# Kernel optimization log

Measured on AMD Instinct MI355X. Metric: run time of the kernel, lower is better.

The kernel has to match this reference:

```python
import jax, jax.numpy as jnp
import numpy as np

N_NODES = 100000
N_EDGES = 3200000
D_IN = 128
D_H0 = 64
D_H1 = 32
N_GRAPHS = 1024
N_CLASSES = 16


def setup_inputs() -> dict:
    key = jax.random.key(0)
    ks = jax.random.split(key, 9)
    x = jax.random.normal(ks[0], (N_NODES, D_IN), dtype=jnp.float32)
    edge_index = jax.random.randint(ks[1], (2, N_EDGES), 0, N_NODES, dtype=jnp.int64)
    node_graph_index = jnp.sort(
        jax.random.randint(ks[2], (N_NODES,), 0, N_GRAPHS, dtype=jnp.int64))

    def glorot(k, shape):
        lim = np.sqrt(6.0 / (shape[0] + shape[1]))
        return jax.random.uniform(k, shape, jnp.float32, -lim, lim)

    W0 = glorot(ks[3], (D_IN, D_H0))
    b0 = jnp.zeros((D_H0,), jnp.float32)
    W1 = glorot(ks[4], (D_H0, D_H1))
    b1 = jnp.zeros((D_H1,), jnp.float32)
    Wd = glorot(ks[5], (D_H1, N_CLASSES))
    bd = jnp.zeros((N_CLASSES,), jnp.float32)
    return {"x": x, "edge_index": edge_index, "node_graph_index": node_graph_index,
            "W0": W0, "b0": b0, "W1": W1, "b1": b1, "Wd": Wd, "bd": bd}


def reference(x, edge_index, node_graph_index, W0, b0, W1, b1, Wd, bd):
    N = x.shape[0]
    # GCN renormalization: add self-loops, symmetric D^-1/2 (A+I) D^-1/2
    loops = jnp.arange(N, dtype=edge_index.dtype)
    row = jnp.concatenate([edge_index[0], loops])  # target nodes
    col = jnp.concatenate([edge_index[1], loops])  # source nodes
    deg = jax.ops.segment_sum(jnp.ones_like(row, dtype=x.dtype), row, num_segments=N)
    inv_sqrt = jax.lax.rsqrt(deg)  # deg >= 1 thanks to self-loops
    norm = inv_sqrt[row] * inv_sqrt[col]  # [E+N]

    def gcn(h, W, b):
        hW = h @ W                                   # [N, d_out]
        msg = hW[col] * norm[:, None]                # [E+N, d_out]
        agg = jax.ops.segment_sum(msg, row, num_segments=N)
        return jax.nn.relu(agg + b)

    h = gcn(x, W0, b0)          # [N, 64]  (dropout is identity at inference)
    h = gcn(h, W1, b1)          # [N, 32]

    # mean pool over graphs
    sums = jax.ops.segment_sum(h, node_graph_index, num_segments=N_GRAPHS)
    cnt = jax.ops.segment_sum(jnp.ones((N,), x.dtype), node_graph_index,
                              num_segments=N_GRAPHS)
    pooled = sums / jnp.maximum(cnt, 1.0)[:, None]   # [G, 32]
    return pooled @ Wd + bd                          # [G, n_classes]
```

## Files before the change

### kernel.cpp

```cpp
#include <hip/hip_runtime.h>

#define GSHIFT 8
#define GSIZE 256
#define MAXG 512
#define GCAP 8960
#define CHUNKA 4096

typedef unsigned short bfraw;

__device__ __forceinline__ bfraw f2bf(float f) {
    unsigned u = __float_as_uint(f);
    unsigned r = u + 0x7FFFu + ((u >> 16) & 1u);
    return (bfraw)(r >> 16);
}
__device__ __forceinline__ float bflo(unsigned u) { return __uint_as_float(u << 16); }
__device__ __forceinline__ float bfhi(unsigned u) { return __uint_as_float(u & 0xFFFF0000u); }


__global__ __launch_bounds__(512) void k_ginit(int* __restrict__ gcur, int ngroups) {
    int g = threadIdx.x;
    if (g < ngroups) gcur[g] = g * GCAP;
}

__global__ __launch_bounds__(512) void k_partA(const int* __restrict__ row,
                                               const int* __restrict__ col,
                                               int* __restrict__ gcur,
                                               int* __restrict__ gbuf,
                                               int E, int ngroups) {
    __shared__ int h[MAXG];
    __shared__ int lst[MAXG];
    __shared__ int base[MAXG];
    __shared__ int sorted[CHUNKA];
    __shared__ int dstIdx[CHUNKA];
    int tid = threadIdx.x;
    h[tid] = 0;
    __syncthreads();
    int start = blockIdx.x * CHUNKA;
    int end = min(E, start + CHUNKA);
    for (int i = start + tid * 4; i < end; i += 2048) {
        if (i + 3 < end) {
            int4 r = *(const int4*)(row + i);
            atomicAdd(&h[r.x >> GSHIFT], 1);
            atomicAdd(&h[r.y >> GSHIFT], 1);
            atomicAdd(&h[r.z >> GSHIFT], 1);
            atomicAdd(&h[r.w >> GSHIFT], 1);
        } else {
            for (int j = i; j < end; ++j) atomicAdd(&h[row[j] >> GSHIFT], 1);
        }
    }
    __syncthreads();
    int v = h[tid];
    lst[tid] = v;
    __syncthreads();
    for (int d = 1; d < MAXG; d <<= 1) {
        int a = (tid >= d) ? lst[tid - d] : 0;
        __syncthreads();
        lst[tid] += a;
        __syncthreads();
    }
    int excl = lst[tid] - v;
    base[tid] = (v > 0 && tid < ngroups) ? atomicAdd(&gcur[tid], v) : 0;
    lst[tid] = excl;
    h[tid] = excl;
    __syncthreads();
    for (int i = start + tid * 4; i < end; i += 2048) {
        if (i + 3 < end) {
            int4 r = *(const int4*)(row + i);
            int4 c = *(const int4*)(col + i);
#pragma unroll
            for (int j = 0; j < 4; ++j) {
                int rr = (&r.x)[j], cc = (&c.x)[j];
                int g = rr >> GSHIFT;
                int p = atomicAdd(&h[g], 1);
                sorted[p] = ((rr & (GSIZE - 1)) << 17) | cc;
                int dst = base[g] + (p - lst[g]);
                dstIdx[p] = (dst < (g + 1) * GCAP) ? dst : -1;
            }
        } else {
            for (int j = i; j < end; ++j) {
                int rr = row[j], cc = col[j];
                int g = rr >> GSHIFT;
                int p = atomicAdd(&h[g], 1);
                sorted[p] = ((rr & (GSIZE - 1)) << 17) | cc;
                int dst = base[g] + (p - lst[g]);
                dstIdx[p] = (dst < (g + 1) * GCAP) ? dst : -1;
            }
        }
    }
    __syncthreads();
    int cnt = end - start;
    for (int i = tid; i < cnt; i += 512) {
        int d = dstIdx[i];
        if (d >= 0) gbuf[d] = sorted[i];
    }
}

__global__ __launch_bounds__(512) void k_partB(const int* __restrict__ gbuf,
                                               const int* __restrict__ gcur,
                                               int* __restrict__ off,
                                               int* __restrict__ off2,
                                               int* __restrict__ scol,
                                               float* __restrict__ invs, int N) {
    __shared__ int hist[GSIZE];
    __shared__ int lex[GSIZE];
    __shared__ int sorted[GCAP];
    int g = blockIdx.x, tid = threadIdx.x;
    int s = g * GCAP;
    int cnt = min(gcur[g] - s, GCAP);
    if (tid < GSIZE) hist[tid] = 0;
    __syncthreads();
    for (int k = tid; k < cnt; k += 512)
        atomicAdd(&hist[gbuf[s + k] >> 17], 1);
    __syncthreads();
    int d0 = (tid < GSIZE) ? hist[tid] : 0;
    if (tid < GSIZE) lex[tid] = d0;
    __syncthreads();
    for (int d = 1; d < GSIZE; d <<= 1) {
        int a = 0;
        if (tid < GSIZE && tid >= d) a = lex[tid - d];
        __syncthreads();
        if (tid < GSIZE) lex[tid] += a;
        __syncthreads();
    }
    if (tid < GSIZE) {
        int excl = lex[tid] - d0;
        int node = (g << GSHIFT) + tid;
        if (node < N) {
            off[node] = s + excl;
            off2[node] = s + excl + d0;
            invs[node] = rsqrtf((float)(d0 + 1));
        }
        hist[tid] = excl;
    }
    __syncthreads();
    for (int k = tid; k < cnt; k += 512) {
        int p = gbuf[s + k];
        int pos = atomicAdd(&hist[p >> 17], 1);
        sorted[pos] = p & 0x1FFFF;
    }
    __syncthreads();
    for (int k = tid; k < cnt; k += 512) scol[s + k] = sorted[k];
}


__global__ __launch_bounds__(256) void k_gemm0(const float* __restrict__ x,
                                               const float* __restrict__ W,
                                               const float* __restrict__ invs,
                                               bfraw* __restrict__ out, int N) {
    __shared__ float sW[128 * 64];
    for (int i = threadIdx.x; i < 2048; i += 256)
        ((float4*)sW)[i] = ((const float4*)W)[i];
    __syncthreads();
    int t = threadIdx.x;
    int tc = t & 15, tr = t >> 4;
    int rbase = blockIdx.x * 64 + tr * 4;
    float acc[4][4] = {};
    int rr[4];
#pragma unroll
    for (int i = 0; i < 4; ++i) rr[i] = min(rbase + i, N - 1);
    for (int k = 0; k < 128; k += 4) {
        float4 wv0 = *(const float4*)&sW[(k + 0) * 64 + tc * 4];
        float4 wv1 = *(const float4*)&sW[(k + 1) * 64 + tc * 4];
        float4 wv2 = *(const float4*)&sW[(k + 2) * 64 + tc * 4];
        float4 wv3 = *(const float4*)&sW[(k + 3) * 64 + tc * 4];
#pragma unroll
        for (int i = 0; i < 4; ++i) {
            float4 xv = *(const float4*)(x + (size_t)rr[i] * 128 + k);
            acc[i][0] = fmaf(xv.x, wv0.x, acc[i][0]);
            acc[i][1] = fmaf(xv.x, wv0.y, acc[i][1]);
            acc[i][2] = fmaf(xv.x, wv0.z, acc[i][2]);
            acc[i][3] = fmaf(xv.x, wv0.w, acc[i][3]);
            acc[i][0] = fmaf(xv.y, wv1.x, acc[i][0]);
            acc[i][1] = fmaf(xv.y, wv1.y, acc[i][1]);
            acc[i][2] = fmaf(xv.y, wv1.z, acc[i][2]);
            acc[i][3] = fmaf(xv.y, wv1.w, acc[i][3]);
            acc[i][0] = fmaf(xv.z, wv2.x, acc[i][0]);
            acc[i][1] = fmaf(xv.z, wv2.y, acc[i][1]);
            acc[i][2] = fmaf(xv.z, wv2.z, acc[i][2]);
            acc[i][3] = fmaf(xv.z, wv2.w, acc[i][3]);
            acc[i][0] = fmaf(xv.w, wv3.x, acc[i][0]);
            acc[i][1] = fmaf(xv.w, wv3.y, acc[i][1]);
            acc[i][2] = fmaf(xv.w, wv3.z, acc[i][2]);
            acc[i][3] = fmaf(xv.w, wv3.w, acc[i][3]);
        }
    }
#pragma unroll
    for (int i = 0; i < 4; ++i) {
        int row = rbase + i;
        if (row < N) {
            float iv = invs[row];
            ushort4 o;
            o.x = f2bf(iv * acc[i][0]);
            o.y = f2bf(iv * acc[i][1]);
            o.z = f2bf(iv * acc[i][2]);
            o.w = f2bf(iv * acc[i][3]);
            *(ushort4*)(out + (size_t)row * 64 + tc * 4) = o;
        }
    }
}

__global__ __launch_bounds__(256) void k_gemm1(const float* __restrict__ h,
                                               const float* __restrict__ W,
                                               const float* __restrict__ invs,
                                               bfraw* __restrict__ out, int N) {
    __shared__ float sW[64 * 32];
    for (int i = threadIdx.x; i < 512; i += 256)
        ((float4*)sW)[i] = ((const float4*)W)[i];
    __syncthreads();
    int t = threadIdx.x;
    int tc = t & 7, tr = t >> 3;
    int rbase = blockIdx.x * 128 + tr * 4;
    float acc[4][4] = {};
    int rr[4];
#pragma unroll
    for (int i = 0; i < 4; ++i) rr[i] = min(rbase + i, N - 1);
    for (int k = 0; k < 64; k += 4) {
        float4 wv0 = *(const float4*)&sW[(k + 0) * 32 + tc * 4];
        float4 wv1 = *(const float4*)&sW[(k + 1) * 32 + tc * 4];
        float4 wv2 = *(const float4*)&sW[(k + 2) * 32 + tc * 4];
        float4 wv3 = *(const float4*)&sW[(k + 3) * 32 + tc * 4];
#pragma unroll
        for (int i = 0; i < 4; ++i) {
            float4 xv = *(const float4*)(h + (size_t)rr[i] * 64 + k);
            acc[i][0] = fmaf(xv.x, wv0.x, acc[i][0]);
            acc[i][1] = fmaf(xv.x, wv0.y, acc[i][1]);
            acc[i][2] = fmaf(xv.x, wv0.z, acc[i][2]);
            acc[i][3] = fmaf(xv.x, wv0.w, acc[i][3]);
            acc[i][0] = fmaf(xv.y, wv1.x, acc[i][0]);
            acc[i][1] = fmaf(xv.y, wv1.y, acc[i][1]);
            acc[i][2] = fmaf(xv.y, wv1.z, acc[i][2]);
            acc[i][3] = fmaf(xv.y, wv1.w, acc[i][3]);
            acc[i][0] = fmaf(xv.z, wv2.x, acc[i][0]);
            acc[i][1] = fmaf(xv.z, wv2.y, acc[i][1]);
            acc[i][2] = fmaf(xv.z, wv2.z, acc[i][2]);
            acc[i][3] = fmaf(xv.z, wv2.w, acc[i][3]);
            acc[i][0] = fmaf(xv.w, wv3.x, acc[i][0]);
            acc[i][1] = fmaf(xv.w, wv3.y, acc[i][1]);
            acc[i][2] = fmaf(xv.w, wv3.z, acc[i][2]);
            acc[i][3] = fmaf(xv.w, wv3.w, acc[i][3]);
        }
    }
#pragma unroll
    for (int i = 0; i < 4; ++i) {
        int row = rbase + i;
        if (row < N) {
            float iv = invs[row];
            ushort4 o;
            o.x = f2bf(iv * acc[i][0]);
            o.y = f2bf(iv * acc[i][1]);
            o.z = f2bf(iv * acc[i][2]);
            o.w = f2bf(iv * acc[i][3]);
            *(ushort4*)(out + (size_t)row * 32 + tc * 4) = o;
        }
    }
}


__global__ __launch_bounds__(256) void k_agg64_w(const int* __restrict__ scol,
                                                 const int* __restrict__ off,
                                                 const int* __restrict__ off2,
                                                 const float* __restrict__ invs,
                                                 const bfraw* __restrict__ hWb,
                                                 const float* __restrict__ bias,
                                                 float* __restrict__ h0, int N) {
    int node = blockIdx.x * 4 + (threadIdx.x >> 6);
    if (node >= N) return;
    int lane = threadIdx.x & 63;
    int fl = lane & 7, sg = lane >> 3;
    int s = off[node], e = off2[node];
    float a[8] = {}, c[8] = {};
    int k = s + sg;
    for (; k + 24 < e; k += 32) {
        int n0 = scol[k], n1 = scol[k + 8], n2 = scol[k + 16], n3 = scol[k + 24];
        uint4 u0 = *(const uint4*)(hWb + (size_t)n0 * 64 + fl * 8);
        uint4 u1 = *(const uint4*)(hWb + (size_t)n1 * 64 + fl * 8);
        uint4 u2 = *(const uint4*)(hWb + (size_t)n2 * 64 + fl * 8);
        uint4 u3 = *(const uint4*)(hWb + (size_t)n3 * 64 + fl * 8);
        a[0] += bflo(u0.x); a[1] += bfhi(u0.x); a[2] += bflo(u0.y); a[3] += bfhi(u0.y);
        a[4] += bflo(u0.z); a[5] += bfhi(u0.z); a[6] += bflo(u0.w); a[7] += bfhi(u0.w);
        c[0] += bflo(u1.x); c[1] += bfhi(u1.x); c[2] += bflo(u1.y); c[3] += bfhi(u1.y);
        c[4] += bflo(u1.z); c[5] += bfhi(u1.z); c[6] += bflo(u1.w); c[7] += bfhi(u1.w);
        a[0] += bflo(u2.x); a[1] += bfhi(u2.x); a[2] += bflo(u2.y); a[3] += bfhi(u2.y);
        a[4] += bflo(u2.z); a[5] += bfhi(u2.z); a[6] += bflo(u2.w); a[7] += bfhi(u2.w);
        c[0] += bflo(u3.x); c[1] += bfhi(u3.x); c[2] += bflo(u3.y); c[3] += bfhi(u3.y);
        c[4] += bflo(u3.z); c[5] += bfhi(u3.z); c[6] += bflo(u3.w); c[7] += bfhi(u3.w);
    }
    for (; k < e; k += 8) {
        uint4 u = *(const uint4*)(hWb + (size_t)scol[k] * 64 + fl * 8);
        a[0] += bflo(u.x); a[1] += bfhi(u.x); a[2] += bflo(u.y); a[3] += bfhi(u.y);
        a[4] += bflo(u.z); a[5] += bfhi(u.z); a[6] += bflo(u.w); a[7] += bfhi(u.w);
    }
#pragma unroll
    for (int j = 0; j < 8; ++j) a[j] += c[j];
#pragma unroll
    for (int m = 8; m < 64; m <<= 1) {
#pragma unroll
        for (int j = 0; j < 8; ++j) a[j] += __shfl_xor(a[j], m, 64);
    }
    if (sg == 0) {
        uint4 u = *(const uint4*)(hWb + (size_t)node * 64 + fl * 8);
        float iv = invs[node];
        int fb = fl * 8;
        float4 o1, o2;
        o1.x = fmaxf(iv * (a[0] + bflo(u.x)) + bias[fb + 0], 0.f);
        o1.y = fmaxf(iv * (a[1] + bfhi(u.x)) + bias[fb + 1], 0.f);
        o1.z = fmaxf(iv * (a[2] + bflo(u.y)) + bias[fb + 2], 0.f);
        o1.w = fmaxf(iv * (a[3] + bfhi(u.y)) + bias[fb + 3], 0.f);
        o2.x = fmaxf(iv * (a[4] + bflo(u.z)) + bias[fb + 4], 0.f);
        o2.y = fmaxf(iv * (a[5] + bfhi(u.z)) + bias[fb + 5], 0.f);
        o2.z = fmaxf(iv * (a[6] + bflo(u.w)) + bias[fb + 6], 0.f);
        o2.w = fmaxf(iv * (a[7] + bfhi(u.w)) + bias[fb + 7], 0.f);
        *(float4*)(h0 + (size_t)node * 64 + fb) = o1;
        *(float4*)(h0 + (size_t)node * 64 + fb + 4) = o2;
    }
}

__global__ __launch_bounds__(256) void k_agg32_w(const int* __restrict__ scol,
                                                 const int* __restrict__ off,
                                                 const int* __restrict__ off2,
                                                 const float* __restrict__ invs,
                                                 const bfraw* __restrict__ hWb,
                                                 const float* __restrict__ bias,
                                                 float* __restrict__ h1, int N) {
    int node = blockIdx.x * 4 + (threadIdx.x >> 6);
    if (node >= N) return;
    int lane = threadIdx.x & 63;
    int fl = lane & 3, sg = lane >> 2;
    int s = off[node], e = off2[node];
    float a[8] = {}, c[8] = {};
    int k = s + sg;
    for (; k + 16 < e; k += 32) {
        int n0 = scol[k], n1 = scol[k + 16];
        uint4 u0 = *(const uint4*)(hWb + (size_t)n0 * 32 + fl * 8);
        uint4 u1 = *(const uint4*)(hWb + (size_t)n1 * 32 + fl * 8);
        a[0] += bflo(u0.x); a[1] += bfhi(u0.x); a[2] += bflo(u0.y); a[3] += bfhi(u0.y);
        a[4] += bflo(u0.z); a[5] += bfhi(u0.z); a[6] += bflo(u0.w); a[7] += bfhi(u0.w);
        c[0] += bflo(u1.x); c[1] += bfhi(u1.x); c[2] += bflo(u1.y); c[3] += bfhi(u1.y);
        c[4] += bflo(u1.z); c[5] += bfhi(u1.z); c[6] += bflo(u1.w); c[7] += bfhi(u1.w);
    }
    for (; k < e; k += 16) {
        uint4 u = *(const uint4*)(hWb + (size_t)scol[k] * 32 + fl * 8);
        a[0] += bflo(u.x); a[1] += bfhi(u.x); a[2] += bflo(u.y); a[3] += bfhi(u.y);
        a[4] += bflo(u.z); a[5] += bfhi(u.z); a[6] += bflo(u.w); a[7] += bfhi(u.w);
    }
#pragma unroll
    for (int j = 0; j < 8; ++j) a[j] += c[j];
#pragma unroll
    for (int m = 4; m < 64; m <<= 1) {
#pragma unroll
        for (int j = 0; j < 8; ++j) a[j] += __shfl_xor(a[j], m, 64);
    }
    if (sg == 0) {
        uint4 u = *(const uint4*)(hWb + (size_t)node * 32 + fl * 8);
        float iv = invs[node];
        int fb = fl * 8;
        float4 o1, o2;
        o1.x = fmaxf(iv * (a[0] + bflo(u.x)) + bias[fb + 0], 0.f);
        o1.y = fmaxf(iv * (a[1] + bfhi(u.x)) + bias[fb + 1], 0.f);
        o1.z = fmaxf(iv * (a[2] + bflo(u.y)) + bias[fb + 2], 0.f);
        o1.w = fmaxf(iv * (a[3] + bfhi(u.y)) + bias[fb + 3], 0.f);
        o2.x = fmaxf(iv * (a[4] + bflo(u.z)) + bias[fb + 4], 0.f);
        o2.y = fmaxf(iv * (a[5] + bfhi(u.z)) + bias[fb + 5], 0.f);
        o2.z = fmaxf(iv * (a[6] + bflo(u.w)) + bias[fb + 6], 0.f);
        o2.w = fmaxf(iv * (a[7] + bfhi(u.w)) + bias[fb + 7], 0.f);
        *(float4*)(h1 + (size_t)node * 32 + fb) = o1;
        *(float4*)(h1 + (size_t)node * 32 + fb + 4) = o2;
    }
}


__global__ __launch_bounds__(256) void k_gbound(const int* __restrict__ gidx,
                                                int* __restrict__ gstart,
                                                int N, int G) {
    int i = blockIdx.x * 256 + threadIdx.x;
    if (i > N) return;
    if (i == 0) {
        int g0 = gidx[0];
        for (int g = 0; g <= g0; ++g) gstart[g] = 0;
    } else if (i == N) {
        int gl = gidx[N - 1];
        for (int g = gl + 1; g <= G; ++g) gstart[g] = N;
    } else {
        int a = gidx[i - 1], b = gidx[i];
        for (int g = a + 1; g <= b; ++g) gstart[g] = i;
    }
}

__global__ __launch_bounds__(256) void k_pool_head(const float* __restrict__ h1,
                                                   const int* __restrict__ gstart,
                                                   const float* __restrict__ Wd,
                                                   const float* __restrict__ bd,
                                                   float* __restrict__ out) {
    int g = blockIdx.x;
    int s = gstart[g], e = gstart[g + 1];
    int tid = threadIdx.x;
    int lane = tid & 63, w = tid >> 6;
    int f = lane & 31, half = lane >> 5;
    float acc = 0.f;
    for (int n = s + w * 2 + half; n < e; n += 8)
        acc += h1[(size_t)n * 32 + f];
    acc += __shfl_xor(acc, 32, 64);
    __shared__ float red[4][32];
    if (half == 0) red[w][f] = acc;
    __syncthreads();
    if (tid < 32) {
        float v = red[0][tid] + red[1][tid] + red[2][tid] + red[3][tid];
        red[0][tid] = v / fmaxf((float)(e - s), 1.0f);
    }
    __syncthreads();
    if (tid < 16) {
        float acc2 = bd[tid];
#pragma unroll
        for (int j = 0; j < 32; ++j)
            acc2 = fmaf(red[0][j], Wd[j * 16 + tid], acc2);
        out[g * 16 + tid] = acc2;
    }
}


static inline size_t align256(size_t v) { return (v + 255) & ~(size_t)255; }

extern "C" void kernel_launch(void* const* d_in, const int* in_sizes, int n_in,
                              void* d_out, int out_size, void* d_ws, size_t ws_size,
                              hipStream_t stream) {
    const float* x   = (const float*)d_in[0];
    const int*  erow = (const int*)d_in[1];
    const int*  gidx = (const int*)d_in[2];
    const float* W0  = (const float*)d_in[3];
    const float* b0  = (const float*)d_in[4];
    const float* W1  = (const float*)d_in[5];
    const float* b1  = (const float*)d_in[6];
    const float* Wd  = (const float*)d_in[7];
    const float* bd  = (const float*)d_in[8];
    float* out = (float*)d_out;

    const int E = in_sizes[1] / 2;
    const int* ecol = erow + E;
    const int N = in_sizes[2];
    const int G = out_size / 16;
    const int ngroups = (N + GSIZE - 1) / GSIZE;
    const int nchunks = (E + CHUNKA - 1) / CHUNKA;
    const size_t SLOTS = (size_t)ngroups * GCAP;

    char* ws = (char*)d_ws;
    size_t oInvs = 0;
    size_t oOff  = align256(oInvs + (size_t)N * 4);
    size_t oOff2 = align256(oOff + (size_t)N * 4);
    size_t oGc   = align256(oOff2 + (size_t)N * 4);
    size_t oScol = align256(oGc + (size_t)MAXG * 4);
    size_t oA    = align256(oScol + SLOTS * 4);
    size_t oB    = align256(oA + (size_t)N * 128);
    size_t oGs   = align256(oB + (size_t)N * 256);

    float* invs   = (float*)(ws + oInvs);
    int*   off    = (int*)(ws + oOff);
    int*   off2   = (int*)(ws + oOff2);
    int*   gcur   = (int*)(ws + oGc);
    int*   scol   = (int*)(ws + oScol);
    bfraw* tabA   = (bfraw*)(ws + oA);
    float* bufB   = (float*)(ws + oB);
    int*   gstart = (int*)(ws + oGs);
    int*   gbuf   = (int*)bufB;
    float* h1     = bufB;

    k_ginit<<<1, 512, 0, stream>>>(gcur, ngroups);
    k_partA<<<nchunks, 512, 0, stream>>>(erow, ecol, gcur, gbuf, E, ngroups);
    k_partB<<<ngroups, 512, 0, stream>>>(gbuf, gcur, off, off2, scol, invs, N);

    k_gbound<<<(N + 256) / 256, 256, 0, stream>>>(gidx, gstart, N, G);

    k_gemm0<<<(N + 63) / 64, 256, 0, stream>>>(x, W0, invs, tabA, N);
    k_agg64_w<<<(N + 3) / 4, 256, 0, stream>>>(scol, off, off2, invs, tabA, b0, bufB, N);

    k_gemm1<<<(N + 127) / 128, 256, 0, stream>>>(bufB, W1, invs, tabA, N);
    k_agg32_w<<<(N + 3) / 4, 256, 0, stream>>>(scol, off, off2, invs, tabA, b1, h1, N);

    k_pool_head<<<G, 256, 0, stream>>>(h1, gstart, Wd, bd, out);
}
```

Baseline: 324.4 us.

## Load edge chunk once into registers in partition pass and drop gbound kernel

The bucketing kernel now reads each edge's row and col once into 16 registers per thread, instead of reading row twice from global memory. It doubles the chunk size, so there are fewer blocks and fewer atomics on the global group cursors. Each element's destination is now recomputed from a 16-bit group tag rather than a stored int index, which saves shared memory. The separate graph-boundary kernel is removed; instead two threads per pooling block binary-search the sorted graph index, saving one launch at the cost of a few serial global reads.

```diff
diff --git a/kernel.cpp b/kernel.cpp
--- a/kernel.cpp
+++ b/kernel.cpp
@@ -4,7 +4,7 @@
 #define GSIZE 256
 #define MAXG 512
 #define GCAP 8960
-#define CHUNKA 4096
+#define CHUNKA 8192
 
 typedef unsigned short bfraw;
 
@@ -31,23 +31,35 @@
     __shared__ int lst[MAXG];
     __shared__ int base[MAXG];
     __shared__ int sorted[CHUNKA];
-    __shared__ int dstIdx[CHUNKA];
+    __shared__ unsigned short gbin[CHUNKA];
     int tid = threadIdx.x;
     h[tid] = 0;
-    __syncthreads();
     int start = blockIdx.x * CHUNKA;
     int end = min(E, start + CHUNKA);
-    for (int i = start + tid * 4; i < end; i += 2048) {
+    int rr[16], cc[16];
+#pragma unroll
+    for (int q = 0; q < 4; ++q) {
+        int i = start + tid * 4 + q * 2048;
         if (i + 3 < end) {
-            int4 r = *(const int4*)(row + i);
-            atomicAdd(&h[r.x >> GSHIFT], 1);
-            atomicAdd(&h[r.y >> GSHIFT], 1);
-            atomicAdd(&h[r.z >> GSHIFT], 1);
-            atomicAdd(&h[r.w >> GSHIFT], 1);
+            int4 r4 = *(const int4*)(row + i);
+            int4 c4 = *(const int4*)(col + i);
+            rr[q * 4 + 0] = r4.x; rr[q * 4 + 1] = r4.y;
+            rr[q * 4 + 2] = r4.z; rr[q * 4 + 3] = r4.w;
+            cc[q * 4 + 0] = c4.x; cc[q * 4 + 1] = c4.y;
+            cc[q * 4 + 2] = c4.z; cc[q * 4 + 3] = c4.w;
         } else {
-            for (int j = i; j < end; ++j) atomicAdd(&h[row[j] >> GSHIFT], 1);
-        }
-    }
+#pragma unroll
+            for (int j = 0; j < 4; ++j) {
+                int idx = i + j;
+                rr[q * 4 + j] = (idx < end) ? row[idx] : -1;
+                cc[q * 4 + j] = (idx < end) ? col[idx] : 0;
+            }
+        }
+    }
+    __syncthreads();
+#pragma unroll
+    for (int j = 0; j < 16; ++j)
+        if (rr[j] >= 0) atomicAdd(&h[rr[j] >> GSHIFT], 1);
     __syncthreads();
     int v = h[tid];
     lst[tid] = v;
@@ -63,35 +75,23 @@
     lst[tid] = excl;
     h[tid] = excl;
     __syncthreads();
-    for (int i = start + tid * 4; i < end; i += 2048) {
-        if (i + 3 < end) {
-            int4 r = *(const int4*)(row + i);
-            int4 c = *(const int4*)(col + i);
-#pragma unroll
-            for (int j = 0; j < 4; ++j) {
-                int rr = (&r.x)[j], cc = (&c.x)[j];
-                int g = rr >> GSHIFT;
-                int p = atomicAdd(&h[g], 1);
-                sorted[p] = ((rr & (GSIZE - 1)) << 17) | cc;
-                int dst = base[g] + (p - lst[g]);
-                dstIdx[p] = (dst < (g + 1) * GCAP) ? dst : -1;
-            }
-        } else {
-            for (int j = i; j < end; ++j) {
-                int rr = row[j], cc = col[j];
-                int g = rr >> GSHIFT;
-                int p = atomicAdd(&h[g], 1);
-                sorted[p] = ((rr & (GSIZE - 1)) << 17) | cc;
-                int dst = base[g] + (p - lst[g]);
-                dstIdx[p] = (dst < (g + 1) * GCAP) ? dst : -1;
-            }
+#pragma unroll
+    for (int j = 0; j < 16; ++j) {
+        int r = rr[j];
+        if (r >= 0) {
+            int g = r >> GSHIFT;
+            int p = atomicAdd(&h[g], 1);
+            sorted[p] = ((r & (GSIZE - 1)) << 17) | cc[j];
+            gbin[p] = (unsigned short)g;
         }
     }
     __syncthreads();
     int cnt = end - start;
     for (int i = tid; i < cnt; i += 512) {
-        int d = dstIdx[i];
-        if (d >= 0) gbuf[d] = sorted[i];
+        int g = gbin[i];
+        int dst = base[g] + (i - lst[g]);
+        if (dst < (g + 1) * GCAP)
+            gbuf[dst] = sorted[i];
     }
 }
 
@@ -369,31 +369,25 @@
 }
 
 
-__global__ __launch_bounds__(256) void k_gbound(const int* __restrict__ gidx,
-                                                int* __restrict__ gstart,
-                                                int N, int G) {
-    int i = blockIdx.x * 256 + threadIdx.x;
-    if (i > N) return;
-    if (i == 0) {
-        int g0 = gidx[0];
-        for (int g = 0; g <= g0; ++g) gstart[g] = 0;
-    } else if (i == N) {
-        int gl = gidx[N - 1];
-        for (int g = gl + 1; g <= G; ++g) gstart[g] = N;
-    } else {
-        int a = gidx[i - 1], b = gidx[i];
-        for (int g = a + 1; g <= b; ++g) gstart[g] = i;
-    }
-}
-
 __global__ __launch_bounds__(256) void k_pool_head(const float* __restrict__ h1,
-                                                   const int* __restrict__ gstart,
+                                                   const int* __restrict__ gidx,
                                                    const float* __restrict__ Wd,
                                                    const float* __restrict__ bd,
-                                                   float* __restrict__ out) {
+                                                   float* __restrict__ out, int N) {
     int g = blockIdx.x;
-    int s = gstart[g], e = gstart[g + 1];
     int tid = threadIdx.x;
+    __shared__ int bound[2];
+    if (tid < 2) {
+        int target = g + tid;
+        int lo = 0, hi = N;
+        while (lo < hi) {
+            int mid = (lo + hi) >> 1;
+            if (gidx[mid] < target) lo = mid + 1; else hi = mid;
+        }
+        bound[tid] = lo;
+    }
+    __syncthreads();
+    int s = bound[0], e = bound[1];
     int lane = tid & 63, w = tid >> 6;
     int f = lane & 31, half = lane >> 5;
     float acc = 0.f;
@@ -450,7 +444,6 @@
     size_t oScol = align256(oGc + (size_t)MAXG * 4);
     size_t oA    = align256(oScol + SLOTS * 4);
     size_t oB    = align256(oA + (size_t)N * 128);
-    size_t oGs   = align256(oB + (size_t)N * 256);
 
     float* invs   = (float*)(ws + oInvs);
     int*   off    = (int*)(ws + oOff);
@@ -459,7 +452,6 @@
     int*   scol   = (int*)(ws + oScol);
     bfraw* tabA   = (bfraw*)(ws + oA);
     float* bufB   = (float*)(ws + oB);
-    int*   gstart = (int*)(ws + oGs);
     int*   gbuf   = (int*)bufB;
     float* h1     = bufB;
 
@@ -467,13 +459,11 @@
     k_partA<<<nchunks, 512, 0, stream>>>(erow, ecol, gcur, gbuf, E, ngroups);
     k_partB<<<ngroups, 512, 0, stream>>>(gbuf, gcur, off, off2, scol, invs, N);
 
-    k_gbound<<<(N + 256) / 256, 256, 0, stream>>>(gidx, gstart, N, G);
-
     k_gemm0<<<(N + 63) / 64, 256, 0, stream>>>(x, W0, invs, tabA, N);
     k_agg64_w<<<(N + 3) / 4, 256, 0, stream>>>(scol, off, off2, invs, tabA, b0, bufB, N);
 
     k_gemm1<<<(N + 127) / 128, 256, 0, stream>>>(bufB, W1, invs, tabA, N);
     k_agg32_w<<<(N + 3) / 4, 256, 0, stream>>>(scol, off, off2, invs, tabA, b1, h1, N);
 
-    k_pool_head<<<G, 256, 0, stream>>>(h1, gstart, Wd, bd, out);
-}
+    k_pool_head<<<G, 256, 0, stream>>>(h1, gidx, Wd, bd, out, N);
+}
```

Measured after the change: 319.6 us. No clear change (-1.5%).
